# Kernel optimization log

Hardware: AMD Instinct MI355X
Metric: run time of the kernel (lower is better)

The kernel has to match this reference:

```python
import jax, jax.numpy as jnp
import numpy as np

PROT_DIM = 128
LIG_DIM = 128
HIDDEN = 128
RBF_DIM = 16
RBF_CUTOFF = 8.0
SIGMA = 4.0
IN_DIM = PROT_DIM + LIG_DIM + 1 + 3 + RBF_DIM  # 276
N_PROT, N_LIG, N_EDGES = 40000, 10000, 1000000


def _mlp(x, w1, b1, w2, b2):
    return jax.nn.silu(x @ w1 + b1) @ w2 + b2


def setup_inputs() -> dict:
    key = jax.random.key(0)
    ks = jax.random.split(key, 16)
    s = 0.02
    return {
        "h_prot": jax.random.normal(ks[0], (N_PROT, PROT_DIM), jnp.float32),
        "h_lig": jax.random.normal(ks[1], (N_LIG, LIG_DIM), jnp.float32),
        "prot_pos": jax.random.normal(ks[2], (N_PROT, 3), jnp.float32),
        "lig_pos": jax.random.normal(ks[3], (N_LIG, 3), jnp.float32),
        "cross_edges": jax.random.randint(ks[4], (2, N_EDGES), 0, N_LIG, jnp.int32),
        "att_w1": jax.random.normal(ks[5], (IN_DIM, HIDDEN), jnp.float32) * s,
        "att_b1": jnp.zeros((HIDDEN,), jnp.float32),
        "att_w2": jax.random.normal(ks[6], (HIDDEN, 1), jnp.float32) * s,
        "att_b2": jnp.zeros((1,), jnp.float32),
        "proj_w1": jax.random.normal(ks[7], (IN_DIM, HIDDEN), jnp.float32) * s,
        "proj_b1": jnp.zeros((HIDDEN,), jnp.float32),
        "proj_w2": jax.random.normal(ks[8], (HIDDEN, LIG_DIM), jnp.float32) * s,
        "proj_b2": jnp.zeros((LIG_DIM,), jnp.float32),
        "ln_gamma": jnp.ones((LIG_DIM,), jnp.float32),
        "ln_beta": jnp.zeros((LIG_DIM,), jnp.float32),
    }


def reference(h_prot, h_lig, prot_pos, lig_pos, cross_edges,
              att_w1, att_b1, att_w2, att_b2,
              proj_w1, proj_b1, proj_w2, proj_b2,
              ln_gamma, ln_beta):
    p_idx, l_idx = cross_edges[0], cross_edges[1]
    n_lig = h_lig.shape[0]

    hp = h_prot[p_idx]            # [E, prot_dim]
    hl = h_lig[l_idx]             # [E, lig_dim]
    diff = lig_pos[l_idx] - prot_pos[p_idx]          # [E, 3]
    dist = jnp.linalg.norm(diff, axis=-1, keepdims=True)  # [E, 1]
    dir_unit = diff / (dist + 1e-8)
    centers = jnp.linspace(0.0, RBF_CUTOFF, RBF_DIM, dtype=dist.dtype)
    gamma = 1.0 / (2.0 * (RBF_CUTOFF / RBF_DIM) ** 2)
    rbf = jnp.exp(-gamma * (dist - centers) ** 2)    # [E, rbf_dim]
    cat = jnp.concatenate([hp, hl, dist, dir_unit, rbf], axis=-1)  # [E, in_dim]

    logits = _mlp(cat, att_w1, att_b1, att_w2, att_b2)[:, 0]  # [E]
    mx = jax.ops.segment_max(logits, l_idx, num_segments=n_lig)
    w = jnp.exp(logits - mx[l_idx])
    denom = jax.ops.segment_sum(w, l_idx, num_segments=n_lig)
    alpha = w / (denom[l_idx] + 1e-9)

    d = dist[:, 0]
    alpha = alpha * jnp.exp(-d * d / (2.0 * SIGMA * SIGMA))  # dist decay

    v = _mlp(cat, proj_w1, proj_b1, proj_w2, proj_b2)  # [E, lig_dim]
    agg = jax.ops.segment_sum(v * alpha[:, None], l_idx, num_segments=n_lig)

    x = h_lig + agg
    mu = jnp.mean(x, axis=-1, keepdims=True)
    var = jnp.var(x, axis=-1, keepdims=True)
    h_l_out = (x - mu) * jax.lax.rsqrt(var + 1e-5) * ln_gamma + ln_beta
    return h_prot, h_l_out
```

## Files before the change

### kernel.cpp

```cpp
#include <hip/hip_runtime.h>
#include <cstdint>


typedef float f2 __attribute__((ext_vector_type(2)));

__device__ __forceinline__ float fast_rcp(float x) { return __builtin_amdgcn_rcpf(x); }
__device__ __forceinline__ float siluf(float x) { return x * fast_rcp(1.0f + __expf(-x)); }
__device__ __forceinline__ f2 mk2(float a, float b) { f2 r; r.x = a; r.y = b; return r; }
__device__ __forceinline__ f2 fma2(f2 a, f2 b, f2 c) { return __builtin_elementwise_fma(a, b, c); }
__device__ __forceinline__ f2 silu2(f2 x) {
  return mk2(x.x * fast_rcp(1.0f + __expf(-x.x)),
             x.y * fast_rcp(1.0f + __expf(-x.y)));
}

__global__ __launch_bounds__(256) void k_prep(
    const float4* __restrict__ hp4, float4* __restrict__ out4, int n4,
    const float* __restrict__ att_w1, const float* __restrict__ proj_w1,
    float* __restrict__ Gq,
    const int* __restrict__ l_idx, int ne, int* __restrict__ counts) {
  int i = blockIdx.x * blockDim.x + threadIdx.x;
  int stride = gridDim.x * blockDim.x;
  for (int j = i; j < n4; j += stride) out4[j] = hp4[j];
  for (int j = i; j < 20 * 256; j += stride) {
    int k = j >> 8, r = j & 255;
    int ln = r >> 2, c = r & 3;
    int d = 2 * ln + (c & 1);
    const float* src = (c < 2) ? att_w1 : proj_w1;
    Gq[j] = src[(256 + k) * 128 + d];
  }
  for (int j = i; j < ne; j += stride) atomicAdd(&counts[l_idx[j]], 1);
}

__global__ __launch_bounds__(256) void k_tables(
    const float* __restrict__ h, int nrows,
    const float* __restrict__ Wa, const float* __restrict__ Wp,
    const float* __restrict__ ba, const float* __restrict__ bp,
    float* __restrict__ TA, float* __restrict__ TP, int interleaved) {
  __shared__ float hT[128 * 8];
  int t = threadIdx.x;
  int row0 = blockIdx.x * 8;
  for (int i = t; i < 1024; i += 256) {
    int r = i >> 7, k = i & 127;
    int gr = row0 + r;
    hT[k * 8 + r] = (gr < nrows) ? h[gr * 128 + k] : 0.0f;
  }
  __syncthreads();
  const float* W = (t < 128) ? Wa : Wp;
  const float* bias = (t < 128) ? ba : bp;
  int d = t & 127;
  float acc[8] = {0, 0, 0, 0, 0, 0, 0, 0};
  for (int k = 0; k < 128; ++k) {
    float w = W[k * 128 + d];
    const float4* h4 = reinterpret_cast<const float4*>(&hT[k * 8]);
    float4 a = h4[0], b = h4[1];
    acc[0] += a.x * w; acc[1] += a.y * w; acc[2] += a.z * w; acc[3] += a.w * w;
    acc[4] += b.x * w; acc[5] += b.y * w; acc[6] += b.z * w; acc[7] += b.w * w;
  }
  float bv = bias ? bias[d] : 0.0f;
  if (interleaved) {
    int pos = ((d >> 1) << 2) + (d & 1) + ((t < 128) ? 0 : 2);
    #pragma unroll
    for (int r = 0; r < 8; ++r) {
      int gr = row0 + r;
      if (gr < nrows) TA[(size_t)gr * 256 + pos] = acc[r] + bv;
    }
  } else {
    float* T = (t < 128) ? TA : TP;
    #pragma unroll
    for (int r = 0; r < 8; ++r) {
      int gr = row0 + r;
      if (gr < nrows) T[(size_t)gr * 128 + d] = acc[r] + bv;
    }
  }
}

__global__ __launch_bounds__(1024) void k_scan(const int* __restrict__ counts,
                                               int* __restrict__ offsets,
                                               int* __restrict__ cursor, int n) {
  __shared__ int tsum[1024];
  int t = threadIdx.x;
  int per = (n + 1023) >> 10;
  int base = t * per;
  int s = 0;
  for (int i = 0; i < per; ++i) {
    int idx = base + i;
    if (idx < n) s += counts[idx];
  }
  tsum[t] = s;
  __syncthreads();
  for (int off = 1; off < 1024; off <<= 1) {
    int v = (t >= off) ? tsum[t - off] : 0;
    __syncthreads();
    tsum[t] += v;
    __syncthreads();
  }
  int run = (t == 0) ? 0 : tsum[t - 1];
  for (int i = 0; i < per; ++i) {
    int idx = base + i;
    if (idx < n) {
      offsets[idx] = run;
      cursor[idx] = run;
      run += counts[idx];
    }
  }
}

__global__ void k_scatter(const int* __restrict__ p_idx, const int* __restrict__ l_idx, int ne,
                          int* __restrict__ cursor, int* __restrict__ sorted_p) {
  int i = blockIdx.x * blockDim.x + threadIdx.x;
  int stride = gridDim.x * blockDim.x;
  for (; i < ne; i += stride) {
    int l = l_idx[i];
    int pos = atomicAdd(&cursor[l], 1);
    sorted_p[pos] = p_idx[i];
  }
}

__global__ __launch_bounds__(256) void k_edge(
    const float* __restrict__ PAPP, const float* __restrict__ Gq,
    const float* __restrict__ LA, const float* __restrict__ LP,
    const float* __restrict__ prot_pos, const float* __restrict__ lig_pos,
    const int* __restrict__ offsets, const int* __restrict__ counts,
    const int* __restrict__ sorted_p,
    const float* __restrict__ att_w2, const float* __restrict__ att_b2,
    const float* __restrict__ proj_w2, const float* __restrict__ proj_b2,
    const float* __restrict__ h_lig, const float* __restrict__ ln_g,
    const float* __restrict__ ln_b,
    float* __restrict__ out, int np_total, int nl_total) {
  __shared__ alignas(16) float geoS[4][64][24];
  __shared__ alignas(16) int pS[4][64];

  int t = threadIdx.x;
  int wave = t >> 6, lane = t & 63;
  int l = blockIdx.x * 4 + wave;
  if (l >= nl_total) return;
  int dd = 2 * lane;

  const float4* Gq4 = reinterpret_cast<const float4*>(Gq);
  float4 G[20];
  #pragma unroll
  for (int k = 0; k < 20; ++k) G[k] = Gq4[k * 64 + lane];

  float2 lav = *reinterpret_cast<const float2*>(&LA[(size_t)l * 128 + dd]);
  float2 lpv = *reinterpret_cast<const float2*>(&LP[(size_t)l * 128 + dd]);
  float2 wav = *reinterpret_cast<const float2*>(&att_w2[dd]);
  f2 lA2 = mk2(lav.x, lav.y);
  f2 lP2 = mk2(lpv.x, lpv.y);
  float wa0 = wav.x, wa1 = wav.y;
  float lx = lig_pos[l * 3 + 0], ly = lig_pos[l * 3 + 1], lz = lig_pos[l * 3 + 2];
  float b2 = att_b2[0];

  int start = offsets[l];
  int cnt = counts[l];
  f2 acc2 = mk2(0.0f, 0.0f);
  float den = 0.0f, gws = 0.0f;

  const float4* PAPP4 = reinterpret_cast<const float4*>(PAPP);

  for (int cbase = 0; cbase < cnt; cbase += 64) {
    int cc = min(64, cnt - cbase);
    if (lane < cc) {
      int p = sorted_p[start + cbase + lane];
      float px = prot_pos[p * 3 + 0], py = prot_pos[p * 3 + 1], pz = prot_pos[p * 3 + 2];
      float dx = lx - px, dy = ly - py, dz = lz - pz;
      float d2r = dx * dx + dy * dy + dz * dz;
      float dist = sqrtf(d2r);
      float inv = fast_rcp(dist + 1e-8f);
      float rb[16];
      #pragma unroll
      for (int j = 0; j < 16; ++j) {
        float c = (8.0f / 15.0f) * (float)j;
        float dv = dist - c;
        rb[j] = __expf(-2.0f * dv * dv);
      }
      float4* dst = reinterpret_cast<float4*>(&geoS[wave][lane][0]);
      dst[0] = make_float4(dist, dx * inv, dy * inv, dz * inv);
      dst[1] = make_float4(rb[0], rb[1], rb[2], rb[3]);
      dst[2] = make_float4(rb[4], rb[5], rb[6], rb[7]);
      dst[3] = make_float4(rb[8], rb[9], rb[10], rb[11]);
      dst[4] = make_float4(rb[12], rb[13], rb[14], rb[15]);
      geoS[wave][lane][20] = __expf(-d2r * (1.0f / 32.0f));
      pS[wave][lane] = p;
    }
    int pA0 = __builtin_amdgcn_readfirstlane(pS[wave][0]);
    int pB0 = __builtin_amdgcn_readfirstlane(pS[wave][cc > 1 ? 1 : 0]);
    float4 tvA = PAPP4[(size_t)pA0 * 64 + lane];
    float4 tvB = PAPP4[(size_t)pB0 * 64 + lane];
    for (int e = 0; e < cc; e += 2) {
      int eB = (e + 1 < cc) ? e + 1 : e;
      float maskB = (e + 1 < cc) ? 1.0f : 0.0f;
      int e2 = e + 2;
      int iA2 = (e2 < cc) ? e2 : 0;
      int iB2 = (e2 + 1 < cc) ? e2 + 1 : 0;
      int pA2 = __builtin_amdgcn_readfirstlane(pS[wave][iA2]);
      int pB2 = __builtin_amdgcn_readfirstlane(pS[wave][iB2]);
      float4 ntA = PAPP4[(size_t)pA2 * 64 + lane];
      float4 ntB = PAPP4[(size_t)pB2 * 64 + lane];

      const float4* gA4 = reinterpret_cast<const float4*>(&geoS[wave][e][0]);
      const float4* gB4 = reinterpret_cast<const float4*>(&geoS[wave][eB][0]);
      f2 aA = lA2, vA = lP2, aB = lA2, vB = lP2;
      #pragma unroll
      for (int k4 = 0; k4 < 5; ++k4) {
        float4 qA = gA4[k4];
        float4 qB = gB4[k4];
        int k = 4 * k4;
        f2 ga, gp;
        ga = mk2(G[k].x, G[k].y);         gp = mk2(G[k].z, G[k].w);
        aA = fma2(mk2(qA.x, qA.x), ga, aA); vA = fma2(mk2(qA.x, qA.x), gp, vA);
        aB = fma2(mk2(qB.x, qB.x), ga, aB); vB = fma2(mk2(qB.x, qB.x), gp, vB);
        ga = mk2(G[k + 1].x, G[k + 1].y); gp = mk2(G[k + 1].z, G[k + 1].w);
        aA = fma2(mk2(qA.y, qA.y), ga, aA); vA = fma2(mk2(qA.y, qA.y), gp, vA);
        aB = fma2(mk2(qB.y, qB.y), ga, aB); vB = fma2(mk2(qB.y, qB.y), gp, vB);
        ga = mk2(G[k + 2].x, G[k + 2].y); gp = mk2(G[k + 2].z, G[k + 2].w);
        aA = fma2(mk2(qA.z, qA.z), ga, aA); vA = fma2(mk2(qA.z, qA.z), gp, vA);
        aB = fma2(mk2(qB.z, qB.z), ga, aB); vB = fma2(mk2(qB.z, qB.z), gp, vB);
        ga = mk2(G[k + 3].x, G[k + 3].y); gp = mk2(G[k + 3].z, G[k + 3].w);
        aA = fma2(mk2(qA.w, qA.w), ga, aA); vA = fma2(mk2(qA.w, qA.w), gp, vA);
        aB = fma2(mk2(qB.w, qB.w), ga, aB); vB = fma2(mk2(qB.w, qB.w), gp, vB);
      }
      aA = aA + mk2(tvA.x, tvA.y); vA = vA + mk2(tvA.z, tvA.w);
      aB = aB + mk2(tvB.x, tvB.y); vB = vB + mk2(tvB.z, tvB.w);

      f2 hA = silu2(aA), hB = silu2(aB);
      float partA = hA.x * wa0 + hA.y * wa1;
      float partB = hB.x * wa0 + hB.y * wa1;
      #pragma unroll
      for (int off = 32; off; off >>= 1) {
        partA += __shfl_xor(partA, off);
        partB += __shfl_xor(partB, off);
      }
      float gAv = geoS[wave][e][20];
      float gBv = geoS[wave][eB][20];
      float wAe = __expf(partA + b2);
      float wBe = __expf(partB + b2) * maskB;
      float wgA = wAe * gAv, wgB = wBe * gBv;
      f2 sA = silu2(vA), sB = silu2(vB);
      acc2 = fma2(mk2(wgA, wgA), sA, acc2);
      acc2 = fma2(mk2(wgB, wgB), sB, acc2);
      den += wAe + wBe;
      gws += wgA + wgB;
      tvA = ntA; tvB = ntB;
    }
  }

  float invd = 1.0f / (den + 1e-9f);
  float* accW = &geoS[wave][0][0];
  *reinterpret_cast<float2*>(&accW[dd]) = make_float2(acc2.x * invd, acc2.y * invd);
  const float2* W2_2 = reinterpret_cast<const float2*>(proj_w2);
  float agg0 = 0.0f, agg1 = 0.0f;
  #pragma unroll 4
  for (int k = 0; k < 128; k += 4) {
    float4 av = *reinterpret_cast<const float4*>(&accW[k]);
    float2 w0 = W2_2[(size_t)(k + 0) * 64 + lane];
    float2 w1 = W2_2[(size_t)(k + 1) * 64 + lane];
    float2 w2 = W2_2[(size_t)(k + 2) * 64 + lane];
    float2 w3 = W2_2[(size_t)(k + 3) * 64 + lane];
    agg0 += av.x * w0.x + av.y * w1.x + av.z * w2.x + av.w * w3.x;
    agg1 += av.x * w0.y + av.y * w1.y + av.z * w2.y + av.w * w3.y;
  }
  float gval = gws * invd;
  float2 pb2 = *reinterpret_cast<const float2*>(&proj_b2[dd]);
  float2 hl = *reinterpret_cast<const float2*>(&h_lig[(size_t)l * 128 + dd]);
  float x0 = agg0 + gval * pb2.x + hl.x;
  float x1 = agg1 + gval * pb2.y + hl.y;
  float s = x0 + x1, q = x0 * x0 + x1 * x1;
  #pragma unroll
  for (int off = 32; off; off >>= 1) {
    s += __shfl_xor(s, off);
    q += __shfl_xor(q, off);
  }
  float mu = s * (1.0f / 128.0f);
  float var = q * (1.0f / 128.0f) - mu * mu;
  float rstd = rsqrtf(var + 1e-5f);
  float2 gm = *reinterpret_cast<const float2*>(&ln_g[dd]);
  float2 bt = *reinterpret_cast<const float2*>(&ln_b[dd]);
  float2 y = make_float2((x0 - mu) * rstd * gm.x + bt.x,
                         (x1 - mu) * rstd * gm.y + bt.y);
  *reinterpret_cast<float2*>(&out[(size_t)(np_total + l) * 128 + dd]) = y;
}

extern "C" void kernel_launch(void* const* d_in, const int* in_sizes, int n_in,
                              void* d_out, int out_size, void* d_ws, size_t ws_size,
                              hipStream_t stream) {
  const float* h_prot   = (const float*)d_in[0];
  const float* h_lig    = (const float*)d_in[1];
  const float* prot_pos = (const float*)d_in[2];
  const float* lig_pos  = (const float*)d_in[3];
  const int*   edges    = (const int*)d_in[4];
  const float* att_w1   = (const float*)d_in[5];
  const float* att_b1   = (const float*)d_in[6];
  const float* att_w2   = (const float*)d_in[7];
  const float* att_b2   = (const float*)d_in[8];
  const float* proj_w1  = (const float*)d_in[9];
  const float* proj_b1  = (const float*)d_in[10];
  const float* proj_w2  = (const float*)d_in[11];
  const float* proj_b2  = (const float*)d_in[12];
  const float* ln_g     = (const float*)d_in[13];
  const float* ln_b     = (const float*)d_in[14];

  int NP = in_sizes[0] / 128;
  int NL = in_sizes[1] / 128;
  int NE = in_sizes[4] / 2;
  const int* p_idx = edges;
  const int* l_idx = edges + NE;

  float* out = (float*)d_out;

  float* PAPP = (float*)d_ws;
  float* LA = PAPP + (size_t)NP * 256;
  float* LP = LA + (size_t)NL * 128;
  float* Gq = LP + (size_t)NL * 128;
  int* counts  = (int*)(Gq + 20 * 256);
  int* offsets = counts + NL;
  int* cursor  = offsets + NL;
  int* sorted_p = cursor + NL;

  hipMemsetAsync(counts, 0, (size_t)NL * sizeof(int), stream);

  k_prep<<<2048, 256, 0, stream>>>((const float4*)h_prot, (float4*)out, NP * 128 / 4,
                                   att_w1, proj_w1, Gq, l_idx, NE, counts);

  k_tables<<<(NP + 7) / 8, 256, 0, stream>>>(h_prot, NP, att_w1, proj_w1,
                                             nullptr, nullptr, PAPP, nullptr, 1);
  k_tables<<<(NL + 7) / 8, 256, 0, stream>>>(h_lig, NL, att_w1 + 128 * 128,
                                             proj_w1 + 128 * 128, att_b1, proj_b1,
                                             LA, LP, 0);

  k_scan<<<1, 1024, 0, stream>>>(counts, offsets, cursor, NL);
  k_scatter<<<4096, 256, 0, stream>>>(p_idx, l_idx, NE, cursor, sorted_p);

  k_edge<<<(NL + 3) / 4, 256, 0, stream>>>(PAPP, Gq, LA, LP, prot_pos, lig_pos,
                                           offsets, counts, sorted_p,
                                           att_w2, att_b2, proj_w2, proj_b2,
                                           h_lig, ln_g, ln_b, out, NP, NL);
}
```

Baseline: 569.3 us.

## Restructure edge loop: one edge per iteration, DPP wave reductions, register-held edge data

The edge inner loop now processes one edge per iteration instead of two. The 20-wide geometry dot product is split into packed FMAs over pairs of k, using a reorganised Gq layout with 40 float2 rows. Wave reductions switch from shfl_xor butterflies to DPP row adds plus four readlanes. The per-edge protein index and decay weight live in registers and are read with readlane instead of through shared memory. This cuts LDS traffic and shuffle latency, but it loses the two-edge ILP and shortens the prefetch distance to one edge.

```diff
diff --git a/kernel.cpp b/kernel.cpp
--- a/kernel.cpp
+++ b/kernel.cpp
@@ -3,14 +3,27 @@
 
 
 typedef float f2 __attribute__((ext_vector_type(2)));
+typedef float f4 __attribute__((ext_vector_type(4)));
 
 __device__ __forceinline__ float fast_rcp(float x) { return __builtin_amdgcn_rcpf(x); }
 __device__ __forceinline__ float siluf(float x) { return x * fast_rcp(1.0f + __expf(-x)); }
-__device__ __forceinline__ f2 mk2(float a, float b) { f2 r; r.x = a; r.y = b; return r; }
 __device__ __forceinline__ f2 fma2(f2 a, f2 b, f2 c) { return __builtin_elementwise_fma(a, b, c); }
-__device__ __forceinline__ f2 silu2(f2 x) {
-  return mk2(x.x * fast_rcp(1.0f + __expf(-x.x)),
-             x.y * fast_rcp(1.0f + __expf(-x.y)));
+
+template <int CTRL>
+__device__ __forceinline__ float dpp_add(float x) {
+  int t = __builtin_amdgcn_update_dpp(0, __builtin_bit_cast(int, x), CTRL, 0xF, 0xF, true);
+  return x + __builtin_bit_cast(float, t);
+}
+__device__ __forceinline__ float rdlane(float x, int lane) {
+  return __builtin_bit_cast(float, __builtin_amdgcn_readlane(__builtin_bit_cast(int, x), lane));
+}
+__device__ __forceinline__ float wave_sum(float x) {
+  x = dpp_add<0xB1>(x);
+  x = dpp_add<0x4E>(x);
+  x = dpp_add<0x141>(x);
+  x = dpp_add<0x140>(x);
+  float a = rdlane(x, 0), b = rdlane(x, 16), c = rdlane(x, 32), d = rdlane(x, 48);
+  return (a + b) + (c + d);
 }
 
 __global__ __launch_bounds__(256) void k_prep(
@@ -21,12 +34,12 @@
   int i = blockIdx.x * blockDim.x + threadIdx.x;
   int stride = gridDim.x * blockDim.x;
   for (int j = i; j < n4; j += stride) out4[j] = hp4[j];
-  for (int j = i; j < 20 * 256; j += stride) {
-    int k = j >> 8, r = j & 255;
-    int ln = r >> 2, c = r & 3;
-    int d = 2 * ln + (c & 1);
-    const float* src = (c < 2) ? att_w1 : proj_w1;
-    Gq[j] = src[(256 + k) * 128 + d];
+  for (int j = i; j < 40 * 128; j += stride) {
+    int r = j >> 7, c = j & 127;
+    int m = r >> 2, grp = r & 3;
+    int lane = c >> 1, half = c & 1;
+    const float* src = (grp < 2) ? att_w1 : proj_w1;
+    Gq[j] = src[(256 + 2 * m + half) * 128 + 2 * lane + (grp & 1)];
   }
   for (int j = i; j < ne; j += stride) atomicAdd(&counts[l_idx[j]], 1);
 }
@@ -127,8 +140,7 @@
     const float* __restrict__ h_lig, const float* __restrict__ ln_g,
     const float* __restrict__ ln_b,
     float* __restrict__ out, int np_total, int nl_total) {
-  __shared__ alignas(16) float geoS[4][64][24];
-  __shared__ alignas(16) int pS[4][64];
+  __shared__ alignas(16) float geoS[4][64][20];
 
   int t = threadIdx.x;
   int wave = t >> 6, lane = t & 63;
@@ -136,31 +148,32 @@
   if (l >= nl_total) return;
   int dd = 2 * lane;
 
-  const float4* Gq4 = reinterpret_cast<const float4*>(Gq);
-  float4 G[20];
+  const f2* Gq2 = reinterpret_cast<const f2*>(Gq);
+  f2 G2[40];
   #pragma unroll
-  for (int k = 0; k < 20; ++k) G[k] = Gq4[k * 64 + lane];
+  for (int r = 0; r < 40; ++r) G2[r] = Gq2[r * 64 + lane];
 
   float2 lav = *reinterpret_cast<const float2*>(&LA[(size_t)l * 128 + dd]);
   float2 lpv = *reinterpret_cast<const float2*>(&LP[(size_t)l * 128 + dd]);
   float2 wav = *reinterpret_cast<const float2*>(&att_w2[dd]);
-  f2 lA2 = mk2(lav.x, lav.y);
-  f2 lP2 = mk2(lpv.x, lpv.y);
+  float la0 = lav.x, la1 = lav.y, lp0 = lpv.x, lp1 = lpv.y;
   float wa0 = wav.x, wa1 = wav.y;
   float lx = lig_pos[l * 3 + 0], ly = lig_pos[l * 3 + 1], lz = lig_pos[l * 3 + 2];
   float b2 = att_b2[0];
 
   int start = offsets[l];
   int cnt = counts[l];
-  f2 acc2 = mk2(0.0f, 0.0f);
-  float den = 0.0f, gws = 0.0f;
+  float acc0 = 0.0f, acc1 = 0.0f, den = 0.0f, gws = 0.0f;
 
   const float4* PAPP4 = reinterpret_cast<const float4*>(PAPP);
 
   for (int cbase = 0; cbase < cnt; cbase += 64) {
     int cc = min(64, cnt - cbase);
+    float gReg = 0.0f;
+    int pReg = 0;
     if (lane < cc) {
       int p = sorted_p[start + cbase + lane];
+      pReg = p;
       float px = prot_pos[p * 3 + 0], py = prot_pos[p * 3 + 1], pz = prot_pos[p * 3 + 2];
       float dx = lx - px, dy = ly - py, dz = lz - pz;
       float d2r = dx * dx + dy * dy + dz * dz;
@@ -173,80 +186,60 @@
         float dv = dist - c;
         rb[j] = __expf(-2.0f * dv * dv);
       }
-      float4* dst = reinterpret_cast<float4*>(&geoS[wave][lane][0]);
-      dst[0] = make_float4(dist, dx * inv, dy * inv, dz * inv);
-      dst[1] = make_float4(rb[0], rb[1], rb[2], rb[3]);
-      dst[2] = make_float4(rb[4], rb[5], rb[6], rb[7]);
-      dst[3] = make_float4(rb[8], rb[9], rb[10], rb[11]);
-      dst[4] = make_float4(rb[12], rb[13], rb[14], rb[15]);
-      geoS[wave][lane][20] = __expf(-d2r * (1.0f / 32.0f));
-      pS[wave][lane] = p;
-    }
-    int pA0 = __builtin_amdgcn_readfirstlane(pS[wave][0]);
-    int pB0 = __builtin_amdgcn_readfirstlane(pS[wave][cc > 1 ? 1 : 0]);
-    float4 tvA = PAPP4[(size_t)pA0 * 64 + lane];
-    float4 tvB = PAPP4[(size_t)pB0 * 64 + lane];
-    for (int e = 0; e < cc; e += 2) {
-      int eB = (e + 1 < cc) ? e + 1 : e;
-      float maskB = (e + 1 < cc) ? 1.0f : 0.0f;
-      int e2 = e + 2;
-      int iA2 = (e2 < cc) ? e2 : 0;
-      int iB2 = (e2 + 1 < cc) ? e2 + 1 : 0;
-      int pA2 = __builtin_amdgcn_readfirstlane(pS[wave][iA2]);
-      int pB2 = __builtin_amdgcn_readfirstlane(pS[wave][iB2]);
-      float4 ntA = PAPP4[(size_t)pA2 * 64 + lane];
-      float4 ntB = PAPP4[(size_t)pB2 * 64 + lane];
-
-      const float4* gA4 = reinterpret_cast<const float4*>(&geoS[wave][e][0]);
-      const float4* gB4 = reinterpret_cast<const float4*>(&geoS[wave][eB][0]);
-      f2 aA = lA2, vA = lP2, aB = lA2, vB = lP2;
+      f4* dst = reinterpret_cast<f4*>(&geoS[wave][lane][0]);
+      f4 w0; w0[0] = dist; w0[1] = dx * inv; w0[2] = dy * inv; w0[3] = dz * inv;
+      f4 w1; w1[0] = rb[0]; w1[1] = rb[1]; w1[2] = rb[2]; w1[3] = rb[3];
+      f4 w2; w2[0] = rb[4]; w2[1] = rb[5]; w2[2] = rb[6]; w2[3] = rb[7];
+      f4 w3; w3[0] = rb[8]; w3[1] = rb[9]; w3[2] = rb[10]; w3[3] = rb[11];
+      f4 w4; w4[0] = rb[12]; w4[1] = rb[13]; w4[2] = rb[14]; w4[3] = rb[15];
+      dst[0] = w0; dst[1] = w1; dst[2] = w2; dst[3] = w3; dst[4] = w4;
+      gReg = __expf(-d2r * (1.0f / 32.0f));
+    }
+    int p0 = __builtin_amdgcn_readlane(pReg, 0);
+    float4 tv = PAPP4[(size_t)p0 * 64 + lane];
+    for (int e = 0; e < cc; ++e) {
+      int en = (e + 1 < cc) ? e + 1 : e;
+      int pn = __builtin_amdgcn_readlane(pReg, en);
+      float4 nt = PAPP4[(size_t)pn * 64 + lane];
+
+      const f4* q4 = reinterpret_cast<const f4*>(&geoS[wave][e][0]);
+      f2 cA0 = {0.0f, 0.0f}, cA1 = {0.0f, 0.0f};
+      f2 cP0 = {0.0f, 0.0f}, cP1 = {0.0f, 0.0f};
       #pragma unroll
-      for (int k4 = 0; k4 < 5; ++k4) {
-        float4 qA = gA4[k4];
-        float4 qB = gB4[k4];
-        int k = 4 * k4;
-        f2 ga, gp;
-        ga = mk2(G[k].x, G[k].y);         gp = mk2(G[k].z, G[k].w);
-        aA = fma2(mk2(qA.x, qA.x), ga, aA); vA = fma2(mk2(qA.x, qA.x), gp, vA);
-        aB = fma2(mk2(qB.x, qB.x), ga, aB); vB = fma2(mk2(qB.x, qB.x), gp, vB);
-        ga = mk2(G[k + 1].x, G[k + 1].y); gp = mk2(G[k + 1].z, G[k + 1].w);
-        aA = fma2(mk2(qA.y, qA.y), ga, aA); vA = fma2(mk2(qA.y, qA.y), gp, vA);
-        aB = fma2(mk2(qB.y, qB.y), ga, aB); vB = fma2(mk2(qB.y, qB.y), gp, vB);
-        ga = mk2(G[k + 2].x, G[k + 2].y); gp = mk2(G[k + 2].z, G[k + 2].w);
-        aA = fma2(mk2(qA.z, qA.z), ga, aA); vA = fma2(mk2(qA.z, qA.z), gp, vA);
-        aB = fma2(mk2(qB.z, qB.z), ga, aB); vB = fma2(mk2(qB.z, qB.z), gp, vB);
-        ga = mk2(G[k + 3].x, G[k + 3].y); gp = mk2(G[k + 3].z, G[k + 3].w);
-        aA = fma2(mk2(qA.w, qA.w), ga, aA); vA = fma2(mk2(qA.w, qA.w), gp, vA);
-        aB = fma2(mk2(qB.w, qB.w), ga, aB); vB = fma2(mk2(qB.w, qB.w), gp, vB);
+      for (int j = 0; j < 5; ++j) {
+        f4 q = q4[j];
+        f2 qlo = __builtin_shufflevector(q, q, 0, 1);
+        f2 qhi = __builtin_shufflevector(q, q, 2, 3);
+        cA0 = fma2(qlo, G2[8 * j + 0], cA0);
+        cA1 = fma2(qlo, G2[8 * j + 1], cA1);
+        cP0 = fma2(qlo, G2[8 * j + 2], cP0);
+        cP1 = fma2(qlo, G2[8 * j + 3], cP1);
+        cA0 = fma2(qhi, G2[8 * j + 4], cA0);
+        cA1 = fma2(qhi, G2[8 * j + 5], cA1);
+        cP0 = fma2(qhi, G2[8 * j + 6], cP0);
+        cP1 = fma2(qhi, G2[8 * j + 7], cP1);
       }
-      aA = aA + mk2(tvA.x, tvA.y); vA = vA + mk2(tvA.z, tvA.w);
-      aB = aB + mk2(tvB.x, tvB.y); vB = vB + mk2(tvB.z, tvB.w);
-
-      f2 hA = silu2(aA), hB = silu2(aB);
-      float partA = hA.x * wa0 + hA.y * wa1;
-      float partB = hB.x * wa0 + hB.y * wa1;
-      #pragma unroll
-      for (int off = 32; off; off >>= 1) {
-        partA += __shfl_xor(partA, off);
-        partB += __shfl_xor(partB, off);
-      }
-      float gAv = geoS[wave][e][20];
-      float gBv = geoS[wave][eB][20];
-      float wAe = __expf(partA + b2);
-      float wBe = __expf(partB + b2) * maskB;
-      float wgA = wAe * gAv, wgB = wBe * gBv;
-      f2 sA = silu2(vA), sB = silu2(vB);
-      acc2 = fma2(mk2(wgA, wgA), sA, acc2);
-      acc2 = fma2(mk2(wgB, wgB), sB, acc2);
-      den += wAe + wBe;
-      gws += wgA + wgB;
-      tvA = ntA; tvB = ntB;
+      float a0 = (cA0.x + cA0.y) + (la0 + tv.x);
+      float a1 = (cA1.x + cA1.y) + (la1 + tv.y);
+      float pp0 = (cP0.x + cP0.y) + (lp0 + tv.z);
+      float pp1 = (cP1.x + cP1.y) + (lp1 + tv.w);
+
+      float part = siluf(a0) * wa0 + siluf(a1) * wa1;
+      float tot = wave_sum(part);
+      float w = __expf(tot + b2);
+      float g = rdlane(gReg, e);
+      float wg = w * g;
+      acc0 = fmaf(wg, siluf(pp0), acc0);
+      acc1 = fmaf(wg, siluf(pp1), acc1);
+      den += w;
+      gws += wg;
+      tv = nt;
     }
   }
 
   float invd = 1.0f / (den + 1e-9f);
   float* accW = &geoS[wave][0][0];
-  *reinterpret_cast<float2*>(&accW[dd]) = make_float2(acc2.x * invd, acc2.y * invd);
+  *reinterpret_cast<float2*>(&accW[dd]) = make_float2(acc0 * invd, acc1 * invd);
   const float2* W2_2 = reinterpret_cast<const float2*>(proj_w2);
   float agg0 = 0.0f, agg1 = 0.0f;
   #pragma unroll 4
@@ -265,11 +258,8 @@
   float x0 = agg0 + gval * pb2.x + hl.x;
   float x1 = agg1 + gval * pb2.y + hl.y;
   float s = x0 + x1, q = x0 * x0 + x1 * x1;
-  #pragma unroll
-  for (int off = 32; off; off >>= 1) {
-    s += __shfl_xor(s, off);
-    q += __shfl_xor(q, off);
-  }
+  s = wave_sum(s);
+  q = wave_sum(q);
   float mu = s * (1.0f / 128.0f);
   float var = q * (1.0f / 128.0f) - mu * mu;
   float rstd = rsqrtf(var + 1e-5f);
@@ -311,12 +301,12 @@
   float* LA = PAPP + (size_t)NP * 256;
   float* LP = LA + (size_t)NL * 128;
   float* Gq = LP + (size_t)NL * 128;
-  int* counts  = (int*)(Gq + 20 * 256);
+  int* counts  = (int*)(Gq + 40 * 128);
   int* offsets = counts + NL;
   int* cursor  = offsets + NL;
   int* sorted_p = cursor + NL;
 
-  hipMemsetAsync(counts, 0, (size_t)NL * sizeof(int), stream);
+  (void)hipMemsetAsync(counts, 0, (size_t)NL * sizeof(int), stream);
 
   k_prep<<<2048, 256, 0, stream>>>((const float4*)h_prot, (float4*)out, NP * 128 / 4,
                                    att_w1, proj_w1, Gq, l_idx, NE, counts);
```

Measured after the change: 554.1 us. 2.7% less time.
